# Kernel tuning notes

Hardware: AMD Instinct MI355X
Metric: run time of the kernel (lower is better)

## Reference

```python
import jax, jax.numpy as jnp
import numpy as np

CHUNK = 256
THETA = 10000.0

def rope2d(x):
    # x: (b, h, n, d), d divisible by 4
    b, h, n, d = x.shape
    pad = (-n) % CHUNK
    if pad:
        x = jnp.pad(x, ((0, 0), (0, 0), (0, pad), (0, 0)))
    c = (n + pad) // CHUNK
    x = x.reshape(b, h, c, CHUNK, d)
    inv = 1.0 / THETA ** (jnp.arange(0, d, 4, dtype=jnp.float32) / d)  # (d/4,)
    fl = jnp.arange(CHUNK, dtype=jnp.float32)[:, None] * inv[None, :]  # (l, d/4)
    cos_l, sin_l = jnp.cos(fl), jnp.sin(fl)
    fc = jnp.arange(c, dtype=jnp.float32)[:, None] * inv[None, :]      # (c, d/4)
    cos_c, sin_c = jnp.cos(fc)[:, None, :], jnp.sin(fc)[:, None, :]    # (c, 1, d/4)
    x1, x2, x3, x4 = jnp.split(x, 4, axis=-1)
    r1 = x1 * cos_l - x2 * sin_l
    r2 = x1 * sin_l + x2 * cos_l
    r3 = x3 * cos_c - x4 * sin_c
    r4 = x3 * sin_c + x4 * cos_c
    out = jnp.concatenate([r1, r2, r3, r4], axis=-1).reshape(b, h, c * CHUNK, d)
    return out[:, :, :n]


def setup_inputs():
    key = jax.random.key(0)
    ks = jax.random.split(key, 6)
    dim, heads = 512, 8
    b, n = 2, 2048
    s = 0.02
    return {
        'x': jax.random.normal(ks[0], (b, n, dim), dtype=jnp.float32),
        'w_qkv': jax.random.normal(ks[1], (3 * dim, dim), dtype=jnp.float32) * s,
        'b_qkv': jnp.zeros((3 * dim,), dtype=jnp.float32),
        'w_pre': jax.random.normal(ks[2], (heads, heads), dtype=jnp.float32) * 0.3,
        'w_post': jax.random.normal(ks[3], (heads, heads), dtype=jnp.float32) * 0.3,
        'w_out': jax.random.normal(ks[4], (dim, dim), dtype=jnp.float32) * s,
        'b_out': jnp.zeros((dim,), dtype=jnp.float32),
    }


def reference(x, w_qkv, b_qkv, w_pre, w_post, w_out, b_out):
    b, n, dim = x.shape
    heads = w_pre.shape[0]
    d = dim // heads
    scale = d ** -0.5
    qkv = x @ w_qkv.T + b_qkv                      # (b, n, 3*dim)
    q, k, v = jnp.split(qkv, 3, axis=-1)
    def to_heads(t):
        return t.reshape(b, n, heads, d).transpose(0, 2, 1, 3)  # (b, h, n, d)
    q, k, v = to_heads(q), to_heads(k), to_heads(v)
    q = rope2d(q)
    k = rope2d(k)
    logits = jnp.einsum('bhid,bhjd->bhij', q, k) * scale
    # talking-heads pre-softmax mix (Linear over head dim, no bias)
    logits = jnp.einsum('bhij,gh->bgij', logits, w_pre)
    attn = jax.nn.softmax(logits, axis=-1)
    # post-softmax mix
    attn = jnp.einsum('bhij,gh->bgij', attn, w_post)
    out = jnp.einsum('bhij,bhjd->bhid', attn, v)   # (b, h, n, d)
    out = out.transpose(0, 2, 1, 3).reshape(b, n, dim)
    return out @ w_out.T + b_out
```

## Files before the change

kernel.cpp:

```cpp
#include <hip/hip_runtime.h>
#include <hip/hip_bf16.h>

typedef __attribute__((ext_vector_type(8))) short bf16x8;
typedef __attribute__((ext_vector_type(4))) float f32x4;

#define DEV static __device__ __forceinline__

DEV unsigned short f2bf(float f) {
    union { float f; unsigned int u; } v; v.f = f;
    return (unsigned short)((v.u + 0x7FFFu + ((v.u >> 16) & 1u)) >> 16);
}
DEV float bf2f(unsigned short s) {
    union { unsigned int u; float f; } v; v.u = ((unsigned int)s) << 16; return v.f;
}
DEV bf16x8 ld_bf8(const unsigned short* p) {
    return *reinterpret_cast<const bf16x8*>(p);
}
DEV f32x4 mfma16(bf16x8 a, bf16x8 b, f32x4 c) {
    return __builtin_amdgcn_mfma_f32_16x16x32_bf16(a, b, c, 0, 0, 0);
}
DEV bf16x8 make_wfrag(const float* wmat, int li, int lg, float scale) {
    bf16x8 f = {};
    if (lg == 0 && li < 8) {
        #pragma unroll
        for (int t = 0; t < 8; t++) f[t] = (short)f2bf(wmat[li*8 + t] * scale);
    }
    return f;
}

__global__ void k_cvt(const float* __restrict__ s, unsigned short* __restrict__ d, int n) {
    int i = (blockIdx.x * blockDim.x + threadIdx.x) * 4;
    if (i >= n) return;
    float4 v = *reinterpret_cast<const float4*>(s + i);
    ushort4 o = { f2bf(v.x), f2bf(v.y), f2bf(v.z), f2bf(v.w) };
    *reinterpret_cast<ushort4*>(d + i) = o;
}

__global__ __launch_bounds__(256) void k_qkv(
    const unsigned short* __restrict__ xb, const unsigned short* __restrict__ wb,
    const float* __restrict__ bias,
    unsigned short* __restrict__ Qb, unsigned short* __restrict__ Kb,
    unsigned short* __restrict__ Vt)
{
    __shared__ unsigned short As[64][40];
    __shared__ unsigned short Bs[64][40];
    const int m0 = blockIdx.x * 64, c0 = blockIdx.y * 64;
    const int t = threadIdx.x;
    const int w = t >> 6, lane = t & 63, li = lane & 15, lg = lane >> 4;
    const int wr = w >> 1, wc = w & 1;
    f32x4 acc[2][2] = {};
    const int srow = t >> 2, spart = (t & 3) * 8;
    for (int kt = 0; kt < 512; kt += 32) {
        *reinterpret_cast<uint4*>(&As[srow][spart]) =
            *reinterpret_cast<const uint4*>(&xb[(size_t)(m0 + srow) * 512 + kt + spart]);
        *reinterpret_cast<uint4*>(&Bs[srow][spart]) =
            *reinterpret_cast<const uint4*>(&wb[(size_t)(c0 + srow) * 512 + kt + spart]);
        __syncthreads();
        bf16x8 af[2], bfr[2];
        #pragma unroll
        for (int mf = 0; mf < 2; mf++) af[mf] = ld_bf8(&As[wr*32 + mf*16 + li][lg*8]);
        #pragma unroll
        for (int nf = 0; nf < 2; nf++) bfr[nf] = ld_bf8(&Bs[wc*32 + nf*16 + li][lg*8]);
        #pragma unroll
        for (int mf = 0; mf < 2; mf++)
            #pragma unroll
            for (int nf = 0; nf < 2; nf++)
                acc[mf][nf] = mfma16(af[mf], bfr[nf], acc[mf][nf]);
        __syncthreads();
    }
    const int type = c0 >> 9;
    const int head = (c0 & 511) >> 6;
    const float b0 = bias[c0 + wc*32 + li];
    const float b1 = bias[c0 + wc*32 + 16 + li];
    float invf = 0.f;
    if (type < 2) invf = powf(10000.f, -(float)li * (1.f/16.f));
    #pragma unroll
    for (int mf = 0; mf < 2; mf++) {
        #pragma unroll
        for (int r = 0; r < 4; r++) {
            int grow = m0 + wr*32 + mf*16 + lg*4 + r;
            int tok = grow & 2047, bb = grow >> 11;
            float v0 = acc[mf][0][r] + b0;
            float v1 = acc[mf][1][r] + b1;
            if (type < 2) {
                float ang = (wc == 0 ? (float)(tok & 255) : (float)(tok >> 8)) * invf;
                float s, c;
                sincosf(ang, &s, &c);
                float r0 = v0 * c - v1 * s;
                float r1 = v0 * s + v1 * c;
                unsigned short* dst = (type == 0 ? Qb : Kb);
                size_t base = (((size_t)(bb*8 + head)) * 2048 + tok) * 64 + wc*32 + li;
                dst[base]      = f2bf(r0);
                dst[base + 16] = f2bf(r1);
            } else {
                size_t base = (((size_t)(bb*8 + head)) * 64 + wc*32 + li) * 2048 + tok;
                Vt[base]             = f2bf(v0);
                Vt[base + 16 * 2048] = f2bf(v1);
            }
        }
    }
}

__global__ __launch_bounds__(512, 4) void k_lsum(
    const unsigned short* __restrict__ Qb, const unsigned short* __restrict__ Kb,
    const float* __restrict__ w_pre, float* __restrict__ Lp)
{
    __shared__ unsigned short Lt[8192];
    const int blk = blockIdx.x;
    const int jh = blk & 1, it = (blk >> 1) & 127, bb = blk >> 8;
    const int i0 = it * 16;
    const int tid = threadIdx.x, w = tid >> 6, lane = tid & 63, li = lane & 15, lg = lane >> 4;
    bf16x8 W1f = make_wfrag(w_pre, li, lg, 0.125f);
    const unsigned short* Qp = Qb + (((size_t)(bb*8 + w)) * 2048 + i0 + li) * 64;
    bf16x8 qa0 = ld_bf8(Qp + lg*8), qa1 = ld_bf8(Qp + 32 + lg*8);
    const unsigned short* Kp = Kb + ((size_t)(bb*8 + w)) * 2048 * 64;
    const f32x4 zero = {};
    float lacc0 = 0.f, lacc1 = 0.f;
    for (int t = 0; t < 16; t++) {
        int j0 = jh*1024 + t*64;
        f32x4 sa[4] = {};
        #pragma unroll
        for (int nf = 0; nf < 4; nf++) {
            bf16x8 kf0 = ld_bf8(Kp + (size_t)(j0 + nf*16 + li) * 64 + lg*8);
            bf16x8 kf1 = ld_bf8(Kp + (size_t)(j0 + nf*16 + li) * 64 + 32 + lg*8);
            sa[nf] = mfma16(qa0, kf0, sa[nf]);
            sa[nf] = mfma16(qa1, kf1, sa[nf]);
        }
        #pragma unroll
        for (int nf = 0; nf < 4; nf++)
            #pragma unroll
            for (int r = 0; r < 4; r++)
                Lt[((lg*4 + r)*64 + nf*16 + li)*8 + w] = f2bf(sa[nf][r]);
        __syncthreads();
        #pragma unroll
        for (int x = 0; x < 2; x++) {
            int i = 2*w + x;
            float s = 0.f;
            #pragma unroll
            for (int jj = 0; jj < 4; jj++) {
                int e0 = i*64 + jj*16;
                bf16x8 af = {};
                if (lg == 0) af = *(const bf16x8*)&Lt[(e0 + li)*8];
                f32x4 d = mfma16(af, W1f, zero);
                #pragma unroll
                for (int r = 0; r < 4; r++) s += __expf(d[r]);
            }
            if (x == 0) lacc0 += s; else lacc1 += s;
        }
        __syncthreads();
    }
    lacc0 += __shfl_xor(lacc0, 16); lacc0 += __shfl_xor(lacc0, 32);
    lacc1 += __shfl_xor(lacc1, 16); lacc1 += __shfl_xor(lacc1, 32);
    if (li < 8 && lg == 0) {
        float* Lpw = Lp + (size_t)jh * 32768;
        size_t base = (size_t)bb*2048 + i0;
        Lpw[(base + 2*w + 0)*8 + li] = lacc0;
        Lpw[(base + 2*w + 1)*8 + li] = lacc1;
    }
}

__global__ __launch_bounds__(512, 4) void k_attn(
    const unsigned short* __restrict__ Qb, const unsigned short* __restrict__ Kb,
    const unsigned short* __restrict__ Vt,
    const float* __restrict__ w_pre, const float* __restrict__ w_post,
    const float* __restrict__ Lp,
    unsigned short* __restrict__ AOp0, unsigned short* __restrict__ AOp1)
{
    __shared__ unsigned short Lt[8192];
    __shared__ unsigned short Pt[8192];
    __shared__ unsigned short Ah[8 * 1168];
    __shared__ float Llds[128];
    const int blk = blockIdx.x;
    const int jh = blk & 1, it = (blk >> 1) & 127, bb = blk >> 8;
    const int i0 = it * 16;
    const int tid = threadIdx.x, w = tid >> 6, lane = tid & 63, li = lane & 15, lg = lane >> 4;
    bf16x8 W1f = make_wfrag(w_pre, li, lg, 0.125f);
    bf16x8 W2f = make_wfrag(w_post, li, lg, 1.0f);
    if (tid < 128) {
        size_t g = ((size_t)bb*2048 + i0 + (tid >> 3)) * 8 + (tid & 7);
        Llds[tid] = 1.0f / (Lp[g] + Lp[32768 + g]);
    }
    const unsigned short* Qp = Qb + (((size_t)(bb*8 + w)) * 2048 + i0 + li) * 64;
    bf16x8 qa0 = ld_bf8(Qp + lg*8), qa1 = ld_bf8(Qp + 32 + lg*8);
    const unsigned short* Kp = Kb + ((size_t)(bb*8 + w)) * 2048 * 64;
    const unsigned short* Vp = Vt + ((size_t)(bb*8 + w)) * 64 * 2048;
    __syncthreads();
    const int lgc = lg & 1;
    f32x4 invlA = *(const f32x4*)&Llds[(2*w + 0)*8 + lgc*4];
    f32x4 invlB = *(const f32x4*)&Llds[(2*w + 1)*8 + lgc*4];
    const f32x4 zero = {};
    f32x4 oacc[4] = {};
    for (int t = 0; t < 16; t++) {
        int j0 = jh*1024 + t*64;
        f32x4 sa[4] = {};
        #pragma unroll
        for (int nf = 0; nf < 4; nf++) {
            bf16x8 kf0 = ld_bf8(Kp + (size_t)(j0 + nf*16 + li) * 64 + lg*8);
            bf16x8 kf1 = ld_bf8(Kp + (size_t)(j0 + nf*16 + li) * 64 + 32 + lg*8);
            sa[nf] = mfma16(qa0, kf0, sa[nf]);
            sa[nf] = mfma16(qa1, kf1, sa[nf]);
        }
        #pragma unroll
        for (int nf = 0; nf < 4; nf++)
            #pragma unroll
            for (int r = 0; r < 4; r++)
                Lt[((lg*4 + r)*64 + nf*16 + li)*8 + w] = f2bf(sa[nf][r]);
        __syncthreads();
        #pragma unroll
        for (int x = 0; x < 2; x++) {
            int i = 2*w + x;
            f32x4 invl = x ? invlB : invlA;
            #pragma unroll
            for (int jj = 0; jj < 4; jj++) {
                int e0 = i*64 + jj*16;
                bf16x8 bf = {};
                if (lg == 0) bf = *(const bf16x8*)&Lt[(e0 + li)*8];
                f32x4 d = mfma16(W1f, bf, zero);
                if (lg < 2) {
                    unsigned p01 = (unsigned)f2bf(__expf(d[0]) * invl[0])
                                 | ((unsigned)f2bf(__expf(d[1]) * invl[1]) << 16);
                    unsigned p23 = (unsigned)f2bf(__expf(d[2]) * invl[2])
                                 | ((unsigned)f2bf(__expf(d[3]) * invl[3]) << 16);
                    uint2 pk = { p01, p23 };
                    *(uint2*)&Pt[(e0 + li)*8 + lg*4] = pk;
                }
            }
        }
        __syncthreads();
        #pragma unroll
        for (int x = 0; x < 2; x++) {
            int i = 2*w + x;
            #pragma unroll
            for (int jj = 0; jj < 4; jj++) {
                int e0 = i*64 + jj*16;
                bf16x8 af = {};
                if (lg == 0) af = *(const bf16x8*)&Pt[(e0 + li)*8];
                f32x4 d = mfma16(af, W2f, zero);
                if (li < 8) {
                    ushort4 o = { f2bf(d[0]), f2bf(d[1]), f2bf(d[2]), f2bf(d[3]) };
                    *(ushort4*)&Ah[li*1168 + i*72 + jj*16 + lg*4] = o;
                }
            }
        }
        __syncthreads();
        #pragma unroll
        for (int kk = 0; kk < 2; kk++) {
            bf16x8 pa = *(const bf16x8*)&Ah[w*1168 + li*72 + kk*32 + lg*8];
            #pragma unroll
            for (int nf = 0; nf < 4; nf++) {
                bf16x8 vf = ld_bf8(Vp + (size_t)(nf*16 + li) * 2048 + j0 + kk*32 + lg*8);
                oacc[nf] = mfma16(pa, vf, oacc[nf]);
            }
        }
    }
    unsigned short* ao = jh ? AOp1 : AOp0;
    #pragma unroll
    for (int nf = 0; nf < 4; nf++)
        #pragma unroll
        for (int r = 0; r < 4; r++)
            ao[((size_t)bb*2048 + i0 + lg*4 + r)*512 + w*64 + nf*16 + li] = f2bf(oacc[nf][r]);
}

__global__ __launch_bounds__(256) void k_out(
    const unsigned short* __restrict__ a0, const unsigned short* __restrict__ a1,
    const unsigned short* __restrict__ wb, const float* __restrict__ bias,
    float* __restrict__ out)
{
    __shared__ unsigned short As[64][40];
    __shared__ unsigned short Bs[64][40];
    const int m0 = blockIdx.x * 64, c0 = blockIdx.y * 64;
    const int t = threadIdx.x;
    const int w = t >> 6, lane = t & 63, li = lane & 15, lg = lane >> 4;
    const int wr = w >> 1, wc = w & 1;
    f32x4 acc[2][2] = {};
    const int srow = t >> 2, spart = (t & 3) * 8;
    for (int kt = 0; kt < 512; kt += 32) {
        size_t aidx = (size_t)(m0 + srow) * 512 + kt + spart;
        uint4 ua = *(const uint4*)&a0[aidx];
        uint4 ub = *(const uint4*)&a1[aidx];
        const unsigned short* pa = (const unsigned short*)&ua;
        const unsigned short* pb = (const unsigned short*)&ub;
        unsigned short us[8];
        #pragma unroll
        for (int q = 0; q < 8; q++) us[q] = f2bf(bf2f(pa[q]) + bf2f(pb[q]));
        *reinterpret_cast<uint4*>(&As[srow][spart]) = *(const uint4*)us;
        *reinterpret_cast<uint4*>(&Bs[srow][spart]) =
            *reinterpret_cast<const uint4*>(&wb[(size_t)(c0 + srow) * 512 + kt + spart]);
        __syncthreads();
        bf16x8 af[2], bfr[2];
        #pragma unroll
        for (int mf = 0; mf < 2; mf++) af[mf] = ld_bf8(&As[wr*32 + mf*16 + li][lg*8]);
        #pragma unroll
        for (int nf = 0; nf < 2; nf++) bfr[nf] = ld_bf8(&Bs[wc*32 + nf*16 + li][lg*8]);
        #pragma unroll
        for (int mf = 0; mf < 2; mf++)
            #pragma unroll
            for (int nf = 0; nf < 2; nf++)
                acc[mf][nf] = mfma16(af[mf], bfr[nf], acc[mf][nf]);
        __syncthreads();
    }
    #pragma unroll
    for (int mf = 0; mf < 2; mf++)
        #pragma unroll
        for (int nf = 0; nf < 2; nf++)
            #pragma unroll
            for (int r = 0; r < 4; r++) {
                int grow = m0 + wr*32 + mf*16 + lg*4 + r;
                int gcol = c0 + wc*32 + nf*16 + li;
                out[(size_t)grow * 512 + gcol] = acc[mf][nf][r] + bias[gcol];
            }
}

extern "C" void kernel_launch(void* const* d_in, const int* in_sizes, int n_in,
                              void* d_out, int out_size, void* d_ws, size_t ws_size,
                              hipStream_t stream)
{
    const float* x      = (const float*)d_in[0];
    const float* w_qkv  = (const float*)d_in[1];
    const float* b_qkv  = (const float*)d_in[2];
    const float* w_pre  = (const float*)d_in[3];
    const float* w_post = (const float*)d_in[4];
    const float* w_out  = (const float*)d_in[5];
    const float* b_out  = (const float*)d_in[6];
    float* out = (float*)d_out;

    char* ws = (char*)d_ws;
    unsigned short* xb    = (unsigned short*)(ws);
    unsigned short* AOp1  = (unsigned short*)(ws);
    unsigned short* wqkvb = (unsigned short*)(ws + 4194304);
    unsigned short* woutb = (unsigned short*)(ws + 5767168);
    unsigned short* Qb    = (unsigned short*)(ws + 6291456);
    unsigned short* Kb    = (unsigned short*)(ws + 10485760);
    unsigned short* Vt    = (unsigned short*)(ws + 14680064);
    unsigned short* AOp0  = (unsigned short*)(ws + 18874368);
    float* Lp             = (float*)(ws + 23068672);

    k_cvt<<<2048, 256, 0, stream>>>(x, xb, 2097152);
    k_cvt<<<768, 256, 0, stream>>>(w_qkv, wqkvb, 786432);
    k_cvt<<<256, 256, 0, stream>>>(w_out, woutb, 262144);
    k_qkv<<<dim3(64, 24), 256, 0, stream>>>(xb, wqkvb, b_qkv, Qb, Kb, Vt);
    k_lsum<<<512, 512, 0, stream>>>(Qb, Kb, w_pre, Lp);
    k_attn<<<512, 512, 0, stream>>>(Qb, Kb, Vt, w_pre, w_post, Lp, AOp0, AOp1);
    k_out<<<dim3(64, 8), 256, 0, stream>>>(AOp0, AOp1, woutb, b_out, out);
}
```

Measured before the change: 242.3 us.

## Fuse softmax and post-mix via lane shuffles, prefetch V, remap blocks, use exp2

The attention kernel no longer stages normalized probabilities through an LDS buffer. It packs them into the MFMA A-operand by exchanging halves between lanes with a cross-lane shuffle, which removes one LDS round trip and one barrier per tile. V fragments are loaded at the start of each tile so their latency overlaps the QK and mixing work. Both kernels remap block indices so consecutive hardware blocks land on different batch/row groups, fold log2(e) into the pre-mix weights so exp2f can replace __expf, and in k_lsum the barrier is moved to the top of the loop. The shuffle-based operand packing assumes a specific MFMA fragment layout and will give wrong results if that assumption is off.

```diff
diff --git a/kernel.cpp b/kernel.cpp
--- a/kernel.cpp
+++ b/kernel.cpp
@@ -106,26 +106,28 @@
     const float* __restrict__ w_pre, float* __restrict__ Lp)
 {
     __shared__ unsigned short Lt[8192];
-    const int blk = blockIdx.x;
-    const int jh = blk & 1, it = (blk >> 1) & 127, bb = blk >> 8;
+    const int orig = blockIdx.x;
+    const int virt = ((orig & 7) << 6) | (orig >> 3);
+    const int jh = virt & 1, it = (virt >> 1) & 127, bb = virt >> 8;
     const int i0 = it * 16;
     const int tid = threadIdx.x, w = tid >> 6, lane = tid & 63, li = lane & 15, lg = lane >> 4;
-    bf16x8 W1f = make_wfrag(w_pre, li, lg, 0.125f);
+    bf16x8 W1f = make_wfrag(w_pre, li, lg, 0.125f * 1.44269504088896340736f);
     const unsigned short* Qp = Qb + (((size_t)(bb*8 + w)) * 2048 + i0 + li) * 64;
     bf16x8 qa0 = ld_bf8(Qp + lg*8), qa1 = ld_bf8(Qp + 32 + lg*8);
     const unsigned short* Kp = Kb + ((size_t)(bb*8 + w)) * 2048 * 64;
     const f32x4 zero = {};
     float lacc0 = 0.f, lacc1 = 0.f;
+    #pragma unroll 1
     for (int t = 0; t < 16; t++) {
-        int j0 = jh*1024 + t*64;
+        const int j0 = jh*1024 + t*64;
         f32x4 sa[4] = {};
         #pragma unroll
         for (int nf = 0; nf < 4; nf++) {
-            bf16x8 kf0 = ld_bf8(Kp + (size_t)(j0 + nf*16 + li) * 64 + lg*8);
-            bf16x8 kf1 = ld_bf8(Kp + (size_t)(j0 + nf*16 + li) * 64 + 32 + lg*8);
-            sa[nf] = mfma16(qa0, kf0, sa[nf]);
-            sa[nf] = mfma16(qa1, kf1, sa[nf]);
-        }
+            const unsigned short* kp = Kp + (size_t)(j0 + nf*16 + li) * 64;
+            sa[nf] = mfma16(qa0, ld_bf8(kp + lg*8), sa[nf]);
+            sa[nf] = mfma16(qa1, ld_bf8(kp + 32 + lg*8), sa[nf]);
+        }
+        __syncthreads();
         #pragma unroll
         for (int nf = 0; nf < 4; nf++)
             #pragma unroll
@@ -134,24 +136,22 @@
         __syncthreads();
         #pragma unroll
         for (int x = 0; x < 2; x++) {
-            int i = 2*w + x;
+            const int i = 2*w + x;
             float s = 0.f;
             #pragma unroll
             for (int jj = 0; jj < 4; jj++) {
-                int e0 = i*64 + jj*16;
-                bf16x8 af = {};
-                if (lg == 0) af = *(const bf16x8*)&Lt[(e0 + li)*8];
-                f32x4 d = mfma16(af, W1f, zero);
-                #pragma unroll
-                for (int r = 0; r < 4; r++) s += __expf(d[r]);
+                const int e0 = i*64 + jj*16;
+                bf16x8 bfv = {};
+                if (lg == 0) bfv = *(const bf16x8*)&Lt[(e0 + li)*8];
+                f32x4 d = mfma16(bfv, W1f, zero);
+                s += (exp2f(d[0]) + exp2f(d[1])) + (exp2f(d[2]) + exp2f(d[3]));
             }
             if (x == 0) lacc0 += s; else lacc1 += s;
         }
-        __syncthreads();
     }
     lacc0 += __shfl_xor(lacc0, 16); lacc0 += __shfl_xor(lacc0, 32);
     lacc1 += __shfl_xor(lacc1, 16); lacc1 += __shfl_xor(lacc1, 32);
-    if (li < 8 && lg == 0) {
+    if (lg == 0 && li < 8) {
         float* Lpw = Lp + (size_t)jh * 32768;
         size_t base = (size_t)bb*2048 + i0;
         Lpw[(base + 2*w + 0)*8 + li] = lacc0;
@@ -167,14 +167,14 @@
     unsigned short* __restrict__ AOp0, unsigned short* __restrict__ AOp1)
 {
     __shared__ unsigned short Lt[8192];
-    __shared__ unsigned short Pt[8192];
     __shared__ unsigned short Ah[8 * 1168];
     __shared__ float Llds[128];
-    const int blk = blockIdx.x;
-    const int jh = blk & 1, it = (blk >> 1) & 127, bb = blk >> 8;
+    const int orig = blockIdx.x;
+    const int virt = ((orig & 7) << 6) | (orig >> 3);
+    const int jh = virt & 1, it = (virt >> 1) & 127, bb = virt >> 8;
     const int i0 = it * 16;
     const int tid = threadIdx.x, w = tid >> 6, lane = tid & 63, li = lane & 15, lg = lane >> 4;
-    bf16x8 W1f = make_wfrag(w_pre, li, lg, 0.125f);
+    bf16x8 W1f = make_wfrag(w_pre, li, lg, 0.125f * 1.44269504088896340736f);
     bf16x8 W2f = make_wfrag(w_post, li, lg, 1.0f);
     if (tid < 128) {
         size_t g = ((size_t)bb*2048 + i0 + (tid >> 3)) * 8 + (tid & 7);
@@ -190,15 +190,22 @@
     f32x4 invlB = *(const f32x4*)&Llds[(2*w + 1)*8 + lgc*4];
     const f32x4 zero = {};
     f32x4 oacc[4] = {};
+    #pragma unroll 1
     for (int t = 0; t < 16; t++) {
-        int j0 = jh*1024 + t*64;
+        const int j0 = jh*1024 + t*64;
+        bf16x8 vf[8];
+        #pragma unroll
+        for (int nf = 0; nf < 4; nf++) {
+            const unsigned short* vp = Vp + (size_t)(nf*16 + li) * 2048 + j0;
+            vf[nf*2]   = ld_bf8(vp + lg*8);
+            vf[nf*2+1] = ld_bf8(vp + 32 + lg*8);
+        }
         f32x4 sa[4] = {};
         #pragma unroll
         for (int nf = 0; nf < 4; nf++) {
-            bf16x8 kf0 = ld_bf8(Kp + (size_t)(j0 + nf*16 + li) * 64 + lg*8);
-            bf16x8 kf1 = ld_bf8(Kp + (size_t)(j0 + nf*16 + li) * 64 + 32 + lg*8);
-            sa[nf] = mfma16(qa0, kf0, sa[nf]);
-            sa[nf] = mfma16(qa1, kf1, sa[nf]);
+            const unsigned short* kp = Kp + (size_t)(j0 + nf*16 + li) * 64;
+            sa[nf] = mfma16(qa0, ld_bf8(kp + lg*8), sa[nf]);
+            sa[nf] = mfma16(qa1, ld_bf8(kp + 32 + lg*8), sa[nf]);
         }
         #pragma unroll
         for (int nf = 0; nf < 4; nf++)
@@ -208,36 +215,27 @@
         __syncthreads();
         #pragma unroll
         for (int x = 0; x < 2; x++) {
-            int i = 2*w + x;
+            const int i = 2*w + x;
             f32x4 invl = x ? invlB : invlA;
             #pragma unroll
             for (int jj = 0; jj < 4; jj++) {
-                int e0 = i*64 + jj*16;
-                bf16x8 bf = {};
-                if (lg == 0) bf = *(const bf16x8*)&Lt[(e0 + li)*8];
-                f32x4 d = mfma16(W1f, bf, zero);
-                if (lg < 2) {
-                    unsigned p01 = (unsigned)f2bf(__expf(d[0]) * invl[0])
-                                 | ((unsigned)f2bf(__expf(d[1]) * invl[1]) << 16);
-                    unsigned p23 = (unsigned)f2bf(__expf(d[2]) * invl[2])
-                                 | ((unsigned)f2bf(__expf(d[3]) * invl[3]) << 16);
-                    uint2 pk = { p01, p23 };
-                    *(uint2*)&Pt[(e0 + li)*8 + lg*4] = pk;
-                }
-            }
-        }
-        __syncthreads();
-        #pragma unroll
-        for (int x = 0; x < 2; x++) {
-            int i = 2*w + x;
-            #pragma unroll
-            for (int jj = 0; jj < 4; jj++) {
-                int e0 = i*64 + jj*16;
-                bf16x8 af = {};
-                if (lg == 0) af = *(const bf16x8*)&Pt[(e0 + li)*8];
-                f32x4 d = mfma16(af, W2f, zero);
+                const int e0 = i*64 + jj*16;
+                bf16x8 bfv = {};
+                if (lg == 0) bfv = *(const bf16x8*)&Lt[(e0 + li)*8];
+                f32x4 d = mfma16(W1f, bfv, zero);
+                float p0 = exp2f(d[0]) * invl[0];
+                float p1 = exp2f(d[1]) * invl[1];
+                float p2 = exp2f(d[2]) * invl[2];
+                float p3 = exp2f(d[3]) * invl[3];
+                unsigned lo = (unsigned)f2bf(p0) | ((unsigned)f2bf(p1) << 16);
+                unsigned hi = (unsigned)f2bf(p2) | ((unsigned)f2bf(p3) << 16);
+                unsigned plo = (unsigned)__shfl_xor((int)lo, 16);
+                unsigned phi = (unsigned)__shfl_xor((int)hi, 16);
+                union { unsigned u[4]; bf16x8 v; } af;
+                af.u[0] = lo; af.u[1] = hi; af.u[2] = plo; af.u[3] = phi;
+                f32x4 a2 = mfma16(af.v, W2f, zero);
                 if (li < 8) {
-                    ushort4 o = { f2bf(d[0]), f2bf(d[1]), f2bf(d[2]), f2bf(d[3]) };
+                    ushort4 o = { f2bf(a2[0]), f2bf(a2[1]), f2bf(a2[2]), f2bf(a2[3]) };
                     *(ushort4*)&Ah[li*1168 + i*72 + jj*16 + lg*4] = o;
                 }
             }
@@ -247,10 +245,8 @@
         for (int kk = 0; kk < 2; kk++) {
             bf16x8 pa = *(const bf16x8*)&Ah[w*1168 + li*72 + kk*32 + lg*8];
             #pragma unroll
-            for (int nf = 0; nf < 4; nf++) {
-                bf16x8 vf = ld_bf8(Vp + (size_t)(nf*16 + li) * 2048 + j0 + kk*32 + lg*8);
-                oacc[nf] = mfma16(pa, vf, oacc[nf]);
-            }
+            for (int nf = 0; nf < 4; nf++)
+                oacc[nf] = mfma16(pa, vf[nf*2 + kk], oacc[nf]);
         }
     }
     unsigned short* ao = jh ? AOp1 : AOp0;
```

After: 251.0 us. 1.04x slower.
